# Optimization experiments

Hardware: AMD Instinct MI355X
Metric: run time of the kernel (lower is better)

The kernel has to match this reference:

```python
import jax, jax.numpy as jnp
import numpy as np

B, S, T = 8, 2048, 128  # batch, seq_len, token_embedding_dim (== dep_transformed_dim, required by source bug)


def setup_inputs() -> dict:
    key = jax.random.key(0)
    k1, k2, k3, k4, k5, k6, k7 = jax.random.split(key, 7)
    sT = 1.0 / np.sqrt(T)
    sS = 1.0 / np.sqrt(S)
    return {
        "token_embeddings": jax.random.normal(k1, (B, S, T), jnp.float32),
        "dep_embeddings": jax.random.normal(k2, (B, S, T), jnp.float32),  # dead input (source bug), kept for fidelity
        "dep_heads": jax.random.randint(k3, (B, S), 0, S, jnp.int32),
        # composition_transform = Bilinear(T, T, T): weight [T_out, T_in1, T_in2], bias [T_out]
        "W_comp": jax.random.uniform(k4, (T, T, T), jnp.float32, -sT, sT),
        "b_comp": jax.random.uniform(k5, (T,), jnp.float32, -sT, sT),
        # reduction_transform = Linear(S, 1)
        "w_red": jax.random.uniform(k6, (1, S), jnp.float32, -sS, sS),
        "b_red": jax.random.uniform(k7, (1,), jnp.float32, -sS, sS),
    }


def reference(token_embeddings, dep_embeddings, dep_heads, W_comp, b_comp, w_red, b_red):
    # Faithful to source semantics (including the bug where dep_transform output is
    # discarded and tanh is applied to token_embeddings instead):
    #   dense[b,i,j,:] = tanh( bilinear(token[b,j], mask(i==heads[b,j]) * tanh(token[b,j])) )
    #   out[b,i,t]     = sum_j w_red[j] * dense[b,i,j,t] + b_red
    # Where mask is zero, bilinear collapses to its bias, so we never materialize
    # the [B,S,S,T] tensor: compute the 'active' value per token j and scatter-add
    # the delta vs. the bias-only baseline into row i = dep_heads[b,j].
    h = jnp.tanh(token_embeddings)                                   # [B,S,T]
    val = jnp.einsum('bsp,tpq,bsq->bst', token_embeddings, W_comp, h) + b_comp  # [B,S,T]
    act = jnp.tanh(val)                                              # active (masked-in) values
    base_val = jnp.tanh(b_comp)                                      # [T] value where mask is zero
    w = w_red[0]                                                     # [S], reduction weights over j
    base = jnp.sum(w) * base_val + b_red[0]                          # [T] bias-only row
    delta = w[None, :, None] * (act - base_val)                      # [B,S,T]
    b_idx = jnp.arange(token_embeddings.shape[0])[:, None]           # [B,1]
    out = base + jnp.zeros_like(act).at[b_idx, dep_heads].add(delta) # scatter over head rows
    return out
```

## Files before the change

### kernel.cpp

```cpp
#include <hip/hip_runtime.h>
#include <hip/hip_fp16.h>
#include <math.h>

#define S_LEN 2048
#define T_DIM 128
#define BM 128
#define NBLK 256

typedef _Float16 half8 __attribute__((ext_vector_type(8)));
typedef _Float16 half4 __attribute__((ext_vector_type(4)));
typedef float floatx16 __attribute__((ext_vector_type(16)));

__global__ __launch_bounds__(256) void prep_kernel(
    const float* __restrict__ W, const float* __restrict__ w_red,
    const float* __restrict__ b_comp, const float* __restrict__ b_red,
    _Float16* __restrict__ W16f, float* __restrict__ out) {
  const int blk = blockIdx.x;
  const int tid = threadIdx.x;
  if (blk < 256) {
    const int t = blk >> 1, qh = blk & 1;
    const int tc = t >> 5, tl = t & 31;
#pragma unroll
    for (int it = 0; it < 4; ++it) {
      const int e8 = it * 256 + tid;
      const int p = e8 >> 3;
      const int q = qh * 64 + (e8 & 7) * 8;
      const float* src = W + (size_t)t * 16384 + (size_t)p * 128 + q;
      const float4 v0 = *(const float4*)src;
      const float4 v1 = *(const float4*)(src + 4);
      half8 h;
      h[0] = (_Float16)v0.x; h[1] = (_Float16)v0.y;
      h[2] = (_Float16)v0.z; h[3] = (_Float16)v0.w;
      h[4] = (_Float16)v1.x; h[5] = (_Float16)v1.y;
      h[6] = (_Float16)v1.z; h[7] = (_Float16)v1.w;
      const int kc = q >> 4, lh2 = (q >> 3) & 1;
      *(half8*)(W16f + ((size_t)((p * 4 + tc) * 8 + kc)) * 512 + lh2 * 256 + tl * 8) = h;
    }
  } else {
    __shared__ float red4[4];
    float part = 0.f;
#pragma unroll
    for (int i = 0; i < 8; ++i) part += w_red[tid * 8 + i];
#pragma unroll
    for (int off = 32; off > 0; off >>= 1) part += __shfl_down(part, off, 64);
    if ((tid & 63) == 0) red4[tid >> 6] = part;
    __syncthreads();
    const float Sw = red4[0] + red4[1] + red4[2] + red4[3];
    const float br = b_red[0];
    const size_t base = (size_t)(blk - 256) * 1024 + (size_t)tid * 4;
    const int t0 = (int)(base & 127);
    float4 v;
    v.x = Sw * tanhf(b_comp[t0 + 0]) + br;
    v.y = Sw * tanhf(b_comp[t0 + 1]) + br;
    v.z = Sw * tanhf(b_comp[t0 + 2]) + br;
    v.w = Sw * tanhf(b_comp[t0 + 3]) + br;
    *(float4*)(out + base) = v;
  }
}

__global__ __launch_bounds__(512, 2) void main_kernel(
    const float* __restrict__ tok, const int* __restrict__ heads,
    const _Float16* __restrict__ W16f, const float* __restrict__ b_comp,
    const float* __restrict__ w_red, float* __restrict__ out) {
  __shared__ _Float16 tokT2[128 * 128];
  __shared__ float red[128 * 64];

  const int tid = threadIdx.x;
  const int lane = tid & 63;
  const int wave = tid >> 6;
  const int th = wave & 1;
  const int kh = wave >> 1;
  const int l31 = lane & 31;
  const int lh = lane >> 5;
  const int blk = blockIdx.x;
  const int thb = blk & 1;
  const int mb = blk >> 1;
  const size_t tokbase = (size_t)mb * BM * T_DIM;

#pragma unroll
  for (int it = 0; it < 8; ++it) {
    const int f = it * 512 + tid;
    const int m = f >> 5;
    const int p0 = (f & 31) * 4;
    const float4 v = *(const float4*)(tok + tokbase + (size_t)m * 128 + p0);
    const int mi = (m & 31) * 4 + (m >> 5);
    tokT2[(p0 + 0) * 128 + mi] = (_Float16)v.x;
    tokT2[(p0 + 1) * 128 + mi] = (_Float16)v.y;
    tokT2[(p0 + 2) * 128 + mi] = (_Float16)v.z;
    tokT2[(p0 + 3) * 128 + mi] = (_Float16)v.w;
  }

  half8 h16[4][2];
#pragma unroll
  for (int mh = 0; mh < 4; ++mh) {
    const int m = mh * 32 + l31;
#pragma unroll
    for (int ks = 0; ks < 2; ++ks) {
      const int q0 = kh * 32 + ks * 16 + lh * 8;
      const float4 v0 = *(const float4*)(tok + tokbase + (size_t)m * 128 + q0);
      const float4 v1 = *(const float4*)(tok + tokbase + (size_t)m * 128 + q0 + 4);
      h16[mh][ks][0] = (_Float16)tanhf(v0.x);
      h16[mh][ks][1] = (_Float16)tanhf(v0.y);
      h16[mh][ks][2] = (_Float16)tanhf(v0.z);
      h16[mh][ks][3] = (_Float16)tanhf(v0.w);
      h16[mh][ks][4] = (_Float16)tanhf(v1.x);
      h16[mh][ks][5] = (_Float16)tanhf(v1.y);
      h16[mh][ks][6] = (_Float16)tanhf(v1.z);
      h16[mh][ks][7] = (_Float16)tanhf(v1.w);
    }
  }
  __syncthreads();

  const int tc = thb * 2 + th;
  int off0[2];
#pragma unroll
  for (int ks = 0; ks < 2; ++ks)
    off0[ks] = ((tc * 8 + kh * 2 + ks) << 9) + lane * 8;

  floatx16 acc[4];
#pragma unroll
  for (int mh = 0; mh < 4; ++mh)
#pragma unroll
    for (int r = 0; r < 16; ++r) acc[mh][r] = 0.f;

  half8 bf0[2], bf1[2], bf2[2];

  auto loadB = [&](half8 (&bf)[2], int p) {
    const _Float16* wp = W16f + (size_t)p * 16384;
#pragma unroll
    for (int ks = 0; ks < 2; ++ks)
      bf[ks] = *(const half8*)(wp + off0[ks]);
  };

  auto compute = [&](half8 (&bf)[2], int p) {
    const half4 tk = *(const half4*)(tokT2 + p * 128 + l31 * 4);
#pragma unroll
    for (int ks = 0; ks < 2; ++ks) {
      half8 a0 = h16[0][ks] * tk[0];
      half8 a1 = h16[1][ks] * tk[1];
      half8 a2 = h16[2][ks] * tk[2];
      half8 a3 = h16[3][ks] * tk[3];
      acc[0] = __builtin_amdgcn_mfma_f32_32x32x16_f16(a0, bf[ks], acc[0], 0, 0, 0);
      acc[1] = __builtin_amdgcn_mfma_f32_32x32x16_f16(a1, bf[ks], acc[1], 0, 0, 0);
      acc[2] = __builtin_amdgcn_mfma_f32_32x32x16_f16(a2, bf[ks], acc[2], 0, 0, 0);
      acc[3] = __builtin_amdgcn_mfma_f32_32x32x16_f16(a3, bf[ks], acc[3], 0, 0, 0);
    }
  };

  loadB(bf0, 0);
  loadB(bf1, 1);
  for (int p = 0; p < 126; p += 3) {
    loadB(bf2, p + 2);
    compute(bf0, p);
    loadB(bf0, p + 3);
    compute(bf1, p + 1);
    loadB(bf1, p + 4);
    compute(bf2, p + 2);
  }
  compute(bf0, 126);
  compute(bf1, 127);

  __syncthreads();
#pragma unroll
  for (int phase = 0; phase < 4; ++phase) {
    if (kh == phase) {
#pragma unroll
      for (int mh = 0; mh < 4; ++mh)
#pragma unroll
        for (int r = 0; r < 16; ++r) {
          const int m_loc = (r & 3) + 8 * (r >> 2) + 4 * lh;
          const int addr = (mh * 32 + m_loc) * 64 + th * 32 + l31;
          if (phase == 0) red[addr] = acc[mh][r];
          else            red[addr] += acc[mh][r];
        }
    }
    __syncthreads();
  }

  const int t_loc = tid & 63;
  const int mgrp = tid >> 6;
  const int t = thb * 64 + t_loc;
  const float bc = b_comp[t];
  const float tb = tanhf(bc);
#pragma unroll 4
  for (int mi = 0; mi < 16; ++mi) {
    const int m_loc = mi * 8 + mgrp;
    const int gm = mb * BM + m_loc;
    const int head = heads[gm];
    const float wr = w_red[gm & 2047];
    const float v = red[m_loc * 64 + t_loc] + bc;
    atomicAdd(out + ((size_t)(gm >> 11) * S_LEN + head) * T_DIM + t,
              wr * (tanhf(v) - tb));
  }
}

extern "C" void kernel_launch(void* const* d_in, const int* in_sizes, int n_in,
                              void* d_out, int out_size, void* d_ws, size_t ws_size,
                              hipStream_t stream) {
  const float* tok    = (const float*)d_in[0];
  const int*   heads  = (const int*)d_in[2];
  const float* W      = (const float*)d_in[3];
  const float* b_comp = (const float*)d_in[4];
  const float* w_red  = (const float*)d_in[5];
  const float* b_red  = (const float*)d_in[6];
  float* out = (float*)d_out;

  _Float16* W16f = (_Float16*)d_ws;

  prep_kernel<<<2304, 256, 0, stream>>>(W, w_red, b_comp, b_red, W16f, out);
  main_kernel<<<NBLK, 512, 0, stream>>>(tok, heads, W16f, b_comp, w_red, out);
}
```

Before: 169.2 us.

## Split output columns four ways per block to double grid and occupancy

Each block now computes a 32-wide output-column slice instead of 64, which doubles the grid to 512 blocks. Each wave handles a single 16-wide K slice, so per-thread B loads and h16 registers are halved, and launch bounds are raised to 4 blocks per CU. The token transpose tile in shared memory gets a padded row stride to reduce bank conflicts, and the cross-wave reduction uses two partial buffers. The cost is that each block still stages its full token tile and computes tanh for it, so that work is duplicated across the four column slices.

Result: faster. 161.4 us (-4.6%).

```diff
diff --git a/kernel.cpp b/kernel.cpp
--- a/kernel.cpp
+++ b/kernel.cpp
@@ -5,7 +5,9 @@
 #define S_LEN 2048
 #define T_DIM 128
 #define BM 128
-#define NBLK 256
+#define TN 32
+#define NBLK 512
+#define TOKR 132
 
 typedef _Float16 half8 __attribute__((ext_vector_type(8)));
 typedef _Float16 half4 __attribute__((ext_vector_type(4)));
@@ -58,23 +60,21 @@
   }
 }
 
-__global__ __launch_bounds__(512, 2) void main_kernel(
+__global__ __launch_bounds__(512, 4) void main_kernel(
     const float* __restrict__ tok, const int* __restrict__ heads,
     const _Float16* __restrict__ W16f, const float* __restrict__ b_comp,
     const float* __restrict__ w_red, float* __restrict__ out) {
-  __shared__ _Float16 tokT2[128 * 128];
-  __shared__ float red[128 * 64];
+  __shared__ _Float16 tokT2[128 * TOKR];
+  __shared__ float red[2][128 * TN];
 
   const int tid = threadIdx.x;
   const int lane = tid & 63;
-  const int wave = tid >> 6;
-  const int th = wave & 1;
-  const int kh = wave >> 1;
+  const int kh = tid >> 6;
   const int l31 = lane & 31;
   const int lh = lane >> 5;
   const int blk = blockIdx.x;
-  const int thb = blk & 1;
-  const int mb = blk >> 1;
+  const int tq = (blk >> 1) & 3;
+  const int mb = ((blk >> 3) << 1) | (blk & 1);
   const size_t tokbase = (size_t)mb * BM * T_DIM;
 
 #pragma unroll
@@ -84,38 +84,31 @@
     const int p0 = (f & 31) * 4;
     const float4 v = *(const float4*)(tok + tokbase + (size_t)m * 128 + p0);
     const int mi = (m & 31) * 4 + (m >> 5);
-    tokT2[(p0 + 0) * 128 + mi] = (_Float16)v.x;
-    tokT2[(p0 + 1) * 128 + mi] = (_Float16)v.y;
-    tokT2[(p0 + 2) * 128 + mi] = (_Float16)v.z;
-    tokT2[(p0 + 3) * 128 + mi] = (_Float16)v.w;
-  }
-
-  half8 h16[4][2];
+    tokT2[(p0 + 0) * TOKR + mi] = (_Float16)v.x;
+    tokT2[(p0 + 1) * TOKR + mi] = (_Float16)v.y;
+    tokT2[(p0 + 2) * TOKR + mi] = (_Float16)v.z;
+    tokT2[(p0 + 3) * TOKR + mi] = (_Float16)v.w;
+  }
+
+  half8 h16[4];
 #pragma unroll
   for (int mh = 0; mh < 4; ++mh) {
     const int m = mh * 32 + l31;
-#pragma unroll
-    for (int ks = 0; ks < 2; ++ks) {
-      const int q0 = kh * 32 + ks * 16 + lh * 8;
-      const float4 v0 = *(const float4*)(tok + tokbase + (size_t)m * 128 + q0);
-      const float4 v1 = *(const float4*)(tok + tokbase + (size_t)m * 128 + q0 + 4);
-      h16[mh][ks][0] = (_Float16)tanhf(v0.x);
-      h16[mh][ks][1] = (_Float16)tanhf(v0.y);
-      h16[mh][ks][2] = (_Float16)tanhf(v0.z);
-      h16[mh][ks][3] = (_Float16)tanhf(v0.w);
-      h16[mh][ks][4] = (_Float16)tanhf(v1.x);
-      h16[mh][ks][5] = (_Float16)tanhf(v1.y);
-      h16[mh][ks][6] = (_Float16)tanhf(v1.z);
-      h16[mh][ks][7] = (_Float16)tanhf(v1.w);
-    }
+    const int q0 = kh * 16 + lh * 8;
+    const float4 v0 = *(const float4*)(tok + tokbase + (size_t)m * 128 + q0);
+    const float4 v1 = *(const float4*)(tok + tokbase + (size_t)m * 128 + q0 + 4);
+    h16[mh][0] = (_Float16)tanhf(v0.x);
+    h16[mh][1] = (_Float16)tanhf(v0.y);
+    h16[mh][2] = (_Float16)tanhf(v0.z);
+    h16[mh][3] = (_Float16)tanhf(v0.w);
+    h16[mh][4] = (_Float16)tanhf(v1.x);
+    h16[mh][5] = (_Float16)tanhf(v1.y);
+    h16[mh][6] = (_Float16)tanhf(v1.z);
+    h16[mh][7] = (_Float16)tanhf(v1.w);
   }
   __syncthreads();
 
-  const int tc = thb * 2 + th;
-  int off0[2];
-#pragma unroll
-  for (int ks = 0; ks < 2; ++ks)
-    off0[ks] = ((tc * 8 + kh * 2 + ks) << 9) + lane * 8;
+  const int off0 = ((tq * 8 + kh) << 9) + lane * 8;
 
   floatx16 acc[4];
 #pragma unroll
@@ -123,28 +116,22 @@
 #pragma unroll
     for (int r = 0; r < 16; ++r) acc[mh][r] = 0.f;
 
-  half8 bf0[2], bf1[2], bf2[2];
-
-  auto loadB = [&](half8 (&bf)[2], int p) {
-    const _Float16* wp = W16f + (size_t)p * 16384;
-#pragma unroll
-    for (int ks = 0; ks < 2; ++ks)
-      bf[ks] = *(const half8*)(wp + off0[ks]);
+  half8 bf0, bf1, bf2;
+
+  auto loadB = [&](half8& bf, int p) {
+    bf = *(const half8*)(W16f + (size_t)p * 16384 + off0);
   };
 
-  auto compute = [&](half8 (&bf)[2], int p) {
-    const half4 tk = *(const half4*)(tokT2 + p * 128 + l31 * 4);
-#pragma unroll
-    for (int ks = 0; ks < 2; ++ks) {
-      half8 a0 = h16[0][ks] * tk[0];
-      half8 a1 = h16[1][ks] * tk[1];
-      half8 a2 = h16[2][ks] * tk[2];
-      half8 a3 = h16[3][ks] * tk[3];
-      acc[0] = __builtin_amdgcn_mfma_f32_32x32x16_f16(a0, bf[ks], acc[0], 0, 0, 0);
-      acc[1] = __builtin_amdgcn_mfma_f32_32x32x16_f16(a1, bf[ks], acc[1], 0, 0, 0);
-      acc[2] = __builtin_amdgcn_mfma_f32_32x32x16_f16(a2, bf[ks], acc[2], 0, 0, 0);
-      acc[3] = __builtin_amdgcn_mfma_f32_32x32x16_f16(a3, bf[ks], acc[3], 0, 0, 0);
-    }
+  auto compute = [&](half8 bf, int p) {
+    const half4 tk = *(const half4*)(tokT2 + p * TOKR + l31 * 4);
+    half8 a0 = h16[0] * tk[0];
+    half8 a1 = h16[1] * tk[1];
+    half8 a2 = h16[2] * tk[2];
+    half8 a3 = h16[3] * tk[3];
+    acc[0] = __builtin_amdgcn_mfma_f32_32x32x16_f16(a0, bf, acc[0], 0, 0, 0);
+    acc[1] = __builtin_amdgcn_mfma_f32_32x32x16_f16(a1, bf, acc[1], 0, 0, 0);
+    acc[2] = __builtin_amdgcn_mfma_f32_32x32x16_f16(a2, bf, acc[2], 0, 0, 0);
+    acc[3] = __builtin_amdgcn_mfma_f32_32x32x16_f16(a3, bf, acc[3], 0, 0, 0);
   };
 
   loadB(bf0, 0);
@@ -161,34 +148,38 @@
   compute(bf1, 127);
 
   __syncthreads();
-#pragma unroll
-  for (int phase = 0; phase < 4; ++phase) {
-    if (kh == phase) {
-#pragma unroll
-      for (int mh = 0; mh < 4; ++mh)
-#pragma unroll
-        for (int r = 0; r < 16; ++r) {
-          const int m_loc = (r & 3) + 8 * (r >> 2) + 4 * lh;
-          const int addr = (mh * 32 + m_loc) * 64 + th * 32 + l31;
-          if (phase == 0) red[addr] = acc[mh][r];
-          else            red[addr] += acc[mh][r];
-        }
+  {
+    float* R = &red[kh & 1][0];
+    const int g = kh >> 1;
+#pragma unroll
+    for (int phase = 0; phase < 4; ++phase) {
+      if (g == phase) {
+#pragma unroll
+        for (int mh = 0; mh < 4; ++mh)
+#pragma unroll
+          for (int r = 0; r < 16; ++r) {
+            const int m_loc = (r & 3) + 8 * (r >> 2) + 4 * lh;
+            const int addr = (mh * 32 + m_loc) * TN + l31;
+            if (phase == 0) R[addr] = acc[mh][r];
+            else            R[addr] += acc[mh][r];
+          }
+      }
+      __syncthreads();
     }
-    __syncthreads();
-  }
-
-  const int t_loc = tid & 63;
-  const int mgrp = tid >> 6;
-  const int t = thb * 64 + t_loc;
+  }
+
+  const int t_loc = tid & 31;
+  const int mgrp = tid >> 5;
+  const int t = tq * 32 + t_loc;
   const float bc = b_comp[t];
   const float tb = tanhf(bc);
 #pragma unroll 4
-  for (int mi = 0; mi < 16; ++mi) {
-    const int m_loc = mi * 8 + mgrp;
+  for (int mi = 0; mi < 8; ++mi) {
+    const int m_loc = mi * 16 + mgrp;
     const int gm = mb * BM + m_loc;
     const int head = heads[gm];
     const float wr = w_red[gm & 2047];
-    const float v = red[m_loc * 64 + t_loc] + bc;
+    const float v = red[0][m_loc * TN + t_loc] + red[1][m_loc * TN + t_loc] + bc;
     atomicAdd(out + ((size_t)(gm >> 11) * S_LEN + head) * T_DIM + t,
               wr * (tanhf(v) - tb));
   }
```
